# Kernel tuning notes

Hardware: AMD Instinct MI355X
Metric: run time of the kernel (lower is better)

The kernel has to match this reference:

```python
import jax, jax.numpy as jnp
import numpy as np

N_TEST = 16384
NUM_CLASSES = 1000
TEMPERATURE = 2.0


def setup_inputs() -> dict:
    key = jax.random.key(0)
    ks = jax.random.split(key, 6)
    mk = lambda k: jax.random.normal(k, (N_TEST, NUM_CLASSES), dtype=jnp.float32)
    return {
        "outputs1": mk(ks[0]),
        "outputs2": mk(ks[1]),
        "outputs3": mk(ks[2]),
        "outputs4": mk(ks[3]),
        "mimic": mk(ks[4]),
        "targets": jax.random.randint(ks[5], (N_TEST,), 0, NUM_CLASSES, dtype=jnp.int64),
        "n_test": N_TEST,
    }


def _margin(o, targets):
    # top-2 reduction replaces the full descending sort (same top-2 values)
    top2, _ = jax.lax.top_k(o, 2)                                   # [n, 2]
    tgt_val = jnp.take_along_axis(o, targets[:, None], axis=1)[:, 0]  # [n]
    # margin = (max - second_max) only when target is the argmax value, else 0
    return jnp.where(top2[:, 0] == tgt_val, top2[:, 0] - top2[:, 1], jnp.zeros((), o.dtype))


def reference(outputs1, outputs2, outputs3, outputs4, mimic, targets, n_test):
    outs = (outputs1, outputs2, outputs3, outputs4, mimic)
    preds = jnp.stack([_margin(o, targets) for o in outs], axis=1)  # [n, 5]
    out_threshold = jax.nn.softmax(preds / TEMPERATURE, axis=1)
    max_preds = jnp.max(jnp.stack((outputs1, outputs2, outputs3, outputs4), axis=0))
    return max_preds, out_threshold
```

## Files before the change

### kernel.cpp

```cpp
#include <hip/hip_runtime.h>
#include <math.h>

#define NCLS 1000
#define NV4  250
#define INV_TEMP 0.5f
#define NEG_INF (-INFINITY)

__global__ __launch_bounds__(256, 4) void margins_kernel(
    const float* __restrict__ o1, const float* __restrict__ o2,
    const float* __restrict__ o3, const float* __restrict__ o4,
    const float* __restrict__ mim, const int* __restrict__ targets,
    float* __restrict__ out, float* __restrict__ blockmax, int n)
{
    const int lane = threadIdx.x & 63;
    const int wid  = threadIdx.x >> 6;
    const int row  = blockIdx.x * 4 + wid;
    __shared__ float smax[4];

    float gm = NEG_INF;
    const float* mats[5] = {o1, o2, o3, o4, mim};

    if (row < n) {
        const int tgt = targets[row];
        const float4* p4[5];
        #pragma unroll
        for (int m = 0; m < 5; ++m)
            p4[m] = (const float4*)(mats[m] + (size_t)row * NCLS);

        float4 v[5][4];
        #pragma unroll
        for (int it = 0; it < 3; ++it) {
            const int idx = lane + it * 64;
            #pragma unroll
            for (int m = 0; m < 5; ++m) v[m][it] = p4[m][idx];
        }
        {
            const int idx = 192 + lane;
            const int idc = (idx < NV4) ? idx : (NV4 - 1);
            #pragma unroll
            for (int m = 0; m < 5; ++m) v[m][3] = p4[m][idc];
        }
        float tv[5];
        #pragma unroll
        for (int m = 0; m < 5; ++m) tv[m] = ((const float*)p4[m])[tgt];

        if (192 + lane >= NV4) {
            #pragma unroll
            for (int m = 0; m < 5; ++m)
                v[m][3] = make_float4(NEG_INF, NEG_INF, NEG_INF, NEG_INF);
        }

        float preds[5];
        #pragma unroll
        for (int m = 0; m < 5; ++m) {
            float m1 = NEG_INF, m2 = NEG_INF;
            #pragma unroll
            for (int it = 0; it < 4; ++it) {
                const float4 vv = v[m][it];
                const float hi1 = fmaxf(vv.x, vv.y), lo1 = fminf(vv.x, vv.y);
                const float hi2 = fmaxf(vv.z, vv.w), lo2 = fminf(vv.z, vv.w);
                const float t1  = fmaxf(hi1, hi2);
                const float t2  = fmaxf(fminf(hi1, hi2), fmaxf(lo1, lo2));
                m2 = fmaxf(fmaxf(m2, t2), fminf(m1, t1));
                m1 = fmaxf(m1, t1);
                if (m < 4) gm = fmaxf(gm, t1);
            }
            #pragma unroll
            for (int off = 32; off > 0; off >>= 1) {
                const float q1 = __shfl_xor(m1, off, 64);
                const float q2 = __shfl_xor(m2, off, 64);
                m2 = fmaxf(fmaxf(m2, q2), fminf(m1, q1));
                m1 = fmaxf(m1, q1);
            }
            preds[m] = (m1 == tv[m]) ? (m1 - m2) : 0.0f;
        }

        const float p0 = preds[0] * INV_TEMP, p1 = preds[1] * INV_TEMP,
                    p2 = preds[2] * INV_TEMP, p3 = preds[3] * INV_TEMP,
                    p4v = preds[4] * INV_TEMP;
        const float pm = fmaxf(fmaxf(fmaxf(p0, p1), fmaxf(p2, p3)), p4v);
        const float e0 = expf(p0 - pm), e1 = expf(p1 - pm), e2 = expf(p2 - pm),
                    e3 = expf(p3 - pm), e4 = expf(p4v - pm);
        const float inv = 1.0f / (e0 + e1 + e2 + e3 + e4);
        if (lane == 0) {
            float* b = out + 1 + (size_t)row * 5;
            b[0] = e0 * inv; b[1] = e1 * inv; b[2] = e2 * inv;
            b[3] = e3 * inv; b[4] = e4 * inv;
        }
    }

    #pragma unroll
    for (int off = 32; off > 0; off >>= 1)
        gm = fmaxf(gm, __shfl_xor(gm, off, 64));
    if (lane == 0) smax[wid] = gm;
    __syncthreads();
    if (threadIdx.x == 0) {
        blockmax[blockIdx.x] =
            fmaxf(fmaxf(smax[0], smax[1]), fmaxf(smax[2], smax[3]));
    }
}

__global__ __launch_bounds__(256) void final_max_kernel(
    const float* __restrict__ blockmax, int nblocks, float* __restrict__ out)
{
    float m = NEG_INF;
    for (int i = threadIdx.x; i < nblocks; i += 256) m = fmaxf(m, blockmax[i]);
    #pragma unroll
    for (int off = 32; off > 0; off >>= 1)
        m = fmaxf(m, __shfl_xor(m, off, 64));
    __shared__ float s[4];
    const int lane = threadIdx.x & 63, wid = threadIdx.x >> 6;
    if (lane == 0) s[wid] = m;
    __syncthreads();
    if (threadIdx.x == 0)
        out[0] = fmaxf(fmaxf(s[0], s[1]), fmaxf(s[2], s[3]));
}

extern "C" void kernel_launch(void* const* d_in, const int* in_sizes, int n_in,
                              void* d_out, int out_size, void* d_ws, size_t ws_size,
                              hipStream_t stream) {
    const float* o1  = (const float*)d_in[0];
    const float* o2  = (const float*)d_in[1];
    const float* o3  = (const float*)d_in[2];
    const float* o4  = (const float*)d_in[3];
    const float* mim = (const float*)d_in[4];
    const int*   tgt = (const int*)d_in[5];
    const int n = in_sizes[5];

    float* out = (float*)d_out;
    float* ws  = (float*)d_ws;

    const int blocks = (n + 3) / 4;
    margins_kernel<<<blocks, 256, 0, stream>>>(o1, o2, o3, o4, mim, tgt, out, ws, n);
    final_max_kernel<<<1, 256, 0, stream>>>(ws, blocks, out);
}
```

Baseline: 295.0 us.

## Map each row to a 16-lane group and tree-reduce top-2 per lane

```diff
diff --git a/kernel.cpp b/kernel.cpp
--- a/kernel.cpp
+++ b/kernel.cpp
@@ -6,7 +6,13 @@
 #define INV_TEMP 0.5f
 #define NEG_INF (-INFINITY)
 
-__global__ __launch_bounds__(256, 4) void margins_kernel(
+__device__ __forceinline__ void merge2(float& a1, float& a2, float b1, float b2) {
+    const float mn = fminf(a1, b1);
+    a1 = fmaxf(a1, b1);
+    a2 = fmaxf(mn, fmaxf(a2, b2));
+}
+
+__global__ __launch_bounds__(256, 3) void margins_kernel(
     const float* __restrict__ o1, const float* __restrict__ o2,
     const float* __restrict__ o3, const float* __restrict__ o4,
     const float* __restrict__ mim, const int* __restrict__ targets,
@@ -14,7 +20,9 @@
 {
     const int lane = threadIdx.x & 63;
     const int wid  = threadIdx.x >> 6;
-    const int row  = blockIdx.x * 4 + wid;
+    const int grp  = lane >> 4;
+    const int sub  = lane & 15;
+    const int row  = blockIdx.x * 16 + wid * 4 + grp;
     __shared__ float smax[4];
 
     float gm = NEG_INF;
@@ -22,58 +30,59 @@
 
     if (row < n) {
         const int tgt = targets[row];
-        const float4* p4[5];
+
+        float tv[5];
         #pragma unroll
         for (int m = 0; m < 5; ++m)
-            p4[m] = (const float4*)(mats[m] + (size_t)row * NCLS);
+            tv[m] = (mats[m] + (size_t)row * NCLS)[tgt];
 
-        float4 v[5][4];
+        float m1g[5], m2g[5];
         #pragma unroll
-        for (int it = 0; it < 3; ++it) {
-            const int idx = lane + it * 64;
+        for (int m = 0; m < 5; ++m) {
+            const float4* p4 = (const float4*)(mats[m] + (size_t)row * NCLS);
+            float4 v[16];
             #pragma unroll
-            for (int m = 0; m < 5; ++m) v[m][it] = p4[m][idx];
+            for (int it = 0; it < 15; ++it) v[it] = p4[it * 16 + sub];
+            v[15] = p4[(sub < 10) ? (240 + sub) : 249];
+            if (sub >= 10)
+                v[15] = make_float4(NEG_INF, NEG_INF, NEG_INF, NEG_INF);
+
+            float t1[16], t2[16];
+            #pragma unroll
+            for (int it = 0; it < 16; ++it) {
+                const float hi1 = fmaxf(v[it].x, v[it].y), lo1 = fminf(v[it].x, v[it].y);
+                const float hi2 = fmaxf(v[it].z, v[it].w), lo2 = fminf(v[it].z, v[it].w);
+                t1[it] = fmaxf(hi1, hi2);
+                t2[it] = fmaxf(fminf(hi1, hi2), fmaxf(lo1, lo2));
+            }
+            #pragma unroll
+            for (int s = 8; s >= 1; s >>= 1)
+                #pragma unroll
+                for (int i = 0; i < s; ++i)
+                    merge2(t1[i], t2[i], t1[i + s], t2[i + s]);
+
+            m1g[m] = t1[0];
+            m2g[m] = t2[0];
+            if (m < 4) gm = fmaxf(gm, t1[0]);
         }
-        {
-            const int idx = 192 + lane;
-            const int idc = (idx < NV4) ? idx : (NV4 - 1);
+
+        #pragma unroll
+        for (int off = 8; off >= 1; off >>= 1) {
+            float q1[5], q2[5];
             #pragma unroll
-            for (int m = 0; m < 5; ++m) v[m][3] = p4[m][idc];
-        }
-        float tv[5];
-        #pragma unroll
-        for (int m = 0; m < 5; ++m) tv[m] = ((const float*)p4[m])[tgt];
-
-        if (192 + lane >= NV4) {
+            for (int m = 0; m < 5; ++m) {
+                q1[m] = __shfl_xor(m1g[m], off, 64);
+                q2[m] = __shfl_xor(m2g[m], off, 64);
+            }
             #pragma unroll
             for (int m = 0; m < 5; ++m)
-                v[m][3] = make_float4(NEG_INF, NEG_INF, NEG_INF, NEG_INF);
+                merge2(m1g[m], m2g[m], q1[m], q2[m]);
         }
 
         float preds[5];
         #pragma unroll
-        for (int m = 0; m < 5; ++m) {
-            float m1 = NEG_INF, m2 = NEG_INF;
-            #pragma unroll
-            for (int it = 0; it < 4; ++it) {
-                const float4 vv = v[m][it];
-                const float hi1 = fmaxf(vv.x, vv.y), lo1 = fminf(vv.x, vv.y);
-                const float hi2 = fmaxf(vv.z, vv.w), lo2 = fminf(vv.z, vv.w);
-                const float t1  = fmaxf(hi1, hi2);
-                const float t2  = fmaxf(fminf(hi1, hi2), fmaxf(lo1, lo2));
-                m2 = fmaxf(fmaxf(m2, t2), fminf(m1, t1));
-                m1 = fmaxf(m1, t1);
-                if (m < 4) gm = fmaxf(gm, t1);
-            }
-            #pragma unroll
-            for (int off = 32; off > 0; off >>= 1) {
-                const float q1 = __shfl_xor(m1, off, 64);
-                const float q2 = __shfl_xor(m2, off, 64);
-                m2 = fmaxf(fmaxf(m2, q2), fminf(m1, q1));
-                m1 = fmaxf(m1, q1);
-            }
-            preds[m] = (m1 == tv[m]) ? (m1 - m2) : 0.0f;
-        }
+        for (int m = 0; m < 5; ++m)
+            preds[m] = (m1g[m] == tv[m]) ? (m1g[m] - m2g[m]) : 0.0f;
 
         const float p0 = preds[0] * INV_TEMP, p1 = preds[1] * INV_TEMP,
                     p2 = preds[2] * INV_TEMP, p3 = preds[3] * INV_TEMP,
@@ -82,7 +91,7 @@
         const float e0 = expf(p0 - pm), e1 = expf(p1 - pm), e2 = expf(p2 - pm),
                     e3 = expf(p3 - pm), e4 = expf(p4v - pm);
         const float inv = 1.0f / (e0 + e1 + e2 + e3 + e4);
-        if (lane == 0) {
+        if (sub == 0) {
             float* b = out + 1 + (size_t)row * 5;
             b[0] = e0 * inv; b[1] = e1 * inv; b[2] = e2 * inv;
             b[3] = e3 * inv; b[4] = e4 * inv;
@@ -130,7 +139,7 @@
     float* out = (float*)d_out;
     float* ws  = (float*)d_ws;
 
-    const int blocks = (n + 3) / 4;
+    const int blocks = (n + 15) / 16;
     margins_kernel<<<blocks, 256, 0, stream>>>(o1, o2, o3, o4, mim, tgt, out, ws, n);
     final_max_kernel<<<1, 256, 0, stream>>>(ws, blocks, out);
 }
```

Result: no change. 294.8 us (-0.1%).
